# Kernel tuning notes

Measured on AMD Instinct MI355X. Metric: run time of the kernel, lower is better.

The kernel has to match this reference:

```python
import jax, jax.numpy as jnp
import numpy as np
from math import factorial

AGG_NORM = 10.0

def _cg(l1, m1, l2, m2, l3, m3):
    if m3 != m1 + m2:
        return 0.0
    f = factorial
    pre = ((2*l3+1) * f(l3+l1-l2) * f(l3-l1+l2) * f(l1+l2-l3) / f(l1+l2+l3+1)) ** 0.5
    pre *= (f(l3+m3)*f(l3-m3)*f(l1-m1)*f(l1+m1)*f(l2-m2)*f(l2+m2)) ** 0.5
    s = 0.0
    for k in range(0, l1+l2-l3+1):
        d = [k, l1+l2-l3-k, l1-m1-k, l2+m2-k, l3-l2+m1+k, l3-l1-m2+k]
        if min(d) < 0:
            continue
        s += (-1.0)**k / np.prod([float(f(x)) for x in d])
    return pre * s

def _U(l):
    U = np.zeros((2*l+1, 2*l+1), dtype=complex)
    U[l, l] = 1.0
    s2 = 2 ** -0.5
    for m in range(1, l+1):
        U[l+m, l+m] = (-1)**m * s2
        U[l+m, l-m] = s2
        U[l-m, l-m] = 1j * s2
        U[l-m, l+m] = -1j * (-1)**m * s2
    return U

def _real_w3j(l1, l2, l3):
    w = np.zeros((2*l1+1, 2*l2+1, 2*l3+1))
    for m1 in range(-l1, l1+1):
        for m2 in range(-l2, l2+1):
            m3 = -(m1+m2)
            if abs(m3) <= l3:
                w[m1+l1, m2+l2, m3+l3] = (-1.0)**(l1-l2-m3) * _cg(l1, m1, l2, m2, l3, -m3) / (2*l3+1) ** 0.5
    R = np.einsum('im,jn,ko,mno->ijk', _U(l1), _U(l2), _U(l3), w.astype(complex))
    R = R.real if np.abs(R.real).max() >= np.abs(R.imag).max() else R.imag
    return jnp.asarray((R / np.linalg.norm(R)).astype(np.float32))

_TRIPLES = [(0,0,0),(0,1,1),(0,2,2),(1,0,1),(1,1,0),(1,1,2),(1,2,1),(2,0,2),(2,1,1),(2,2,0),(2,2,2),(2,2,4)]
W3J = {t: _real_w3j(*t) for t in _TRIPLES}
PATHS1 = [(0,0,0),(0,1,1),(0,2,2)]
PATHS2 = [(0,0,0),(0,1,1),(0,2,2),(1,0,1),(1,1,0),(1,1,2),(1,2,1),(2,0,2),(2,1,1),(2,2,0),(2,2,2)]
PATHS_P = [(0,0,0),(0,2,2),(2,0,2),(2,2,0),(2,2,2)]
PATHS_4 = [(0,0,0),(2,2,0),(0,2,2),(2,0,2),(2,2,2),(2,2,4)]

def _cart_basis():
    # 21-dim orthonormal basis of rank-4 tensors with ijkl=ijlk=jikl=klij symmetry
    pairs = [(0,0),(1,1),(2,2),(1,2),(0,2),(0,1)]
    mats = []
    for i, j in pairs:
        A = np.zeros((3,3)); A[i,j] = 1.0; A[j,i] = 1.0
        mats.append(A / np.linalg.norm(A))
    B = []
    for a in range(6):
        for b in range(a, 6):
            T = 0.5*(np.einsum('ij,kl->ijkl', mats[a], mats[b]) + np.einsum('ij,kl->ijkl', mats[b], mats[a]))
            B.append(T / np.linalg.norm(T))
    return jnp.asarray(np.stack(B).astype(np.float32))
B21 = _cart_basis()
_MI = np.array([0,1,2,1,0,0]); _MJ = np.array([0,1,2,2,2,1])
_MF = jnp.asarray(np.array([1,1,1,2**0.5,2**0.5,2**0.5], dtype=np.float32))

def _sh(u):
    # component-normalized real spherical harmonics, l=0..2
    x, y, z = u[:,0], u[:,1], u[:,2]
    s0 = jnp.ones_like(x)[:, None]
    s1 = 3**0.5 * u
    s2 = jnp.stack([15**0.5*x*y, 15**0.5*y*z, 5**0.5/2*(3*z*z-1), 15**0.5*x*z, 15**0.5/2*(x*x-y*y)], axis=1)
    return [s0, s1, s2]

def _gauss(x, start, end, n):
    v = jnp.linspace(start, end, n)
    step = (end - start) / (n - 1)
    return jnp.exp(-(((x[:, None] - v) / step) ** 2)) / 1.12

def _lin(x, w):
    return jnp.einsum('nck,cd->ndk', x, w)

def _interaction(xs, sh, ef, senders, receivers, n_nodes, up_w, m1, m2, lin_w, lin_b, paths, norm):
    ups = [None if x is None else _lin(x, up_w[i]) for i, x in enumerate(xs)]
    E = ef.shape[0]
    w = (jax.nn.silu(ef @ m1) @ m2).reshape(E, len(paths), -1)
    gath = {l: ups[l][senders] for l in range(len(ups)) if ups[l] is not None}
    msgs = {}
    for p, (l1, l2, l3) in enumerate(paths):
        m = jnp.einsum('eci,ej,ijk,ec->eck', gath[l1], sh[l2], W3J[(l1, l2, l3)], w[:, p, :])
        msgs[l3] = msgs[l3] + m if l3 in msgs else m
    out = []
    for l in (0, 1, 2):
        agg = jax.ops.segment_sum(msgs[l], receivers, num_segments=n_nodes) / norm
        y = _lin(agg, lin_w[l])
        if l == 0:
            y = y + lin_b[None, :, None]
        out.append(y)
    return out

def _ctp(a, b, pw):
    out = {}
    for p, (l1, l2, l3) in enumerate(PATHS_P):
        m = jnp.einsum('gci,gcj,ijk,c->gck', a[l1], b[l2], W3J[(l1, l2, l3)], pw[p])
        out[l3] = out[l3] + m if l3 in out else m
    return out

def _forward(positions, node_attrs, edge_attr, shifts, W_embed, b_embed, up1_w, mlp1_w1, mlp1_w2, lin1_w, lin1_b, up2_w, mlp2_w1, mlp2_w2, lin2_w, lin2_b, ro_lin_w, ro_gate_w, ro_gate_b, ro_lin2_w, glin_w0, glin_b0, glin_w2, prod_pw2, prod_pw3, prod_lin, fo_w, edge_index, batch, num_graphs):
    N = positions.shape[0]
    senders, receivers = edge_index[0], edge_index[1]
    x0 = (node_attrs @ W_embed + b_embed)[:, :, None]            # [N,64,1]
    vec = positions[receivers] - positions[senders] + shifts
    length = jnp.linalg.norm(vec, axis=1, keepdims=True)
    sh = _sh(vec / (length + 1e-9))
    ef = jnp.concatenate([_gauss(length[:, 0], 0.0, 0.6, 6), _gauss(edge_attr[:, 0], 0.0, 0.03, 6)], axis=1)
    xs = _interaction([x0], sh, ef, senders, receivers, N, up1_w, mlp1_w1, mlp1_w2, lin1_w, lin1_b, PATHS1, AGG_NORM)
    xs = _interaction(xs, sh, ef, senders, receivers, N, up2_w, mlp2_w1, mlp2_w2, lin2_w, lin2_b, PATHS2, AGG_NORM)
    h = [_lin(xs[l], ro_lin_w[l]) for l in range(3)]
    gates = jax.nn.silu(xs[0][:, :, 0] @ ro_gate_w + ro_gate_b)  # [N,128]
    y0 = jax.nn.silu(h[0]); y1 = h[1] * gates[:, :64, None]; y2 = h[2] * gates[:, 64:, None]
    y = [_lin(a, ro_lin2_w[i]) for i, a in enumerate((y0, y1, y2))]
    cnt = jnp.clip(jax.ops.segment_sum(jnp.ones((N,), y[0].dtype), batch, num_segments=num_graphs), 1.0)
    g = [jax.ops.segment_sum(a, batch, num_segments=num_graphs) / cnt[:, None, None] for a in y]
    r = {0: _lin(g[0], glin_w0) + glin_b0[None, :, None], 2: _lin(g[2], glin_w2)}
    t2 = _ctp(r, r, prod_pw2)
    t3 = _ctp(t2, r, prod_pw3)
    r = {l: _lin(r[l], prod_lin[0, i]) + _lin(t2[l], prod_lin[1, i]) + _lin(t3[l], prod_lin[2, i]) for i, l in enumerate((0, 2))}
    outs = {}
    for p, (l1, l2, l3) in enumerate(PATHS_4):
        wp = fo_w[p][:, :, :1] if l3 == 4 else fo_w[p]
        m = jnp.einsum('gui,gvj,ijk,uvw->gwk', r[l1], r[l2], W3J[(l1, l2, l3)], wp)
        outs[l3] = outs[l3] + m if l3 in outs else m
    G = outs[0].shape[0]
    v = jnp.concatenate([outs[0].reshape(G, 2), outs[2].reshape(G, 10), outs[4].reshape(G, 9)], axis=1)
    stiff = jnp.einsum('ga,aijkl->gijkl', v, B21)
    C = stiff[:, _MI[:, None], _MJ[:, None], _MI[None, :], _MJ[None, :]] * (_MF[:, None] * _MF[None, :])
    return C @ C  # matrix_func = 'square'

def setup_inputs():
    k = jax.random.split(jax.random.key(0), 32)
    N, E, G, C = 20000, 200000, 128, 64
    s = lambda i, shape, sc=1.0: jax.random.normal(k[i], shape, dtype=jnp.float32) * sc
    return {
        'positions': jax.random.uniform(k[0], (N, 3), dtype=jnp.float32),
        'node_attrs': jax.random.uniform(k[1], (N, 1), dtype=jnp.float32),
        'edge_attr': jax.random.uniform(k[2], (E, 1), dtype=jnp.float32) * 0.03,
        'shifts': jnp.zeros((E, 3), jnp.float32),
        'W_embed': s(5, (1, C)),
        'b_embed': jnp.zeros((C,), jnp.float32),
        'up1_w': s(6, (1, C, C), C**-0.5),
        'mlp1_w1': s(7, (12, C), 12**-0.5),
        'mlp1_w2': s(8, (C, 3 * C), C**-0.5),
        'lin1_w': s(9, (3, C, C), C**-0.5),
        'lin1_b': jnp.zeros((C,), jnp.float32),
        'up2_w': s(10, (3, C, C), C**-0.5),
        'mlp2_w1': s(11, (12, C), 12**-0.5),
        'mlp2_w2': s(12, (C, 11 * C), C**-0.5),
        'lin2_w': s(13, (3, C, C), C**-0.5),
        'lin2_b': jnp.zeros((C,), jnp.float32),
        'ro_lin_w': s(14, (3, C, C), C**-0.5),
        'ro_gate_w': s(15, (C, 2 * C), C**-0.5),
        'ro_gate_b': jnp.zeros((2 * C,), jnp.float32),
        'ro_lin2_w': s(16, (3, C, C), C**-0.5),
        'glin_w0': s(17, (C, 16), C**-0.5),
        'glin_b0': jnp.zeros((16,), jnp.float32),
        'glin_w2': s(18, (C, 16), C**-0.5),
        'prod_pw2': s(19, (5, 16), 0.5),
        'prod_pw3': s(20, (5, 16), 0.5),
        'prod_lin': s(21, (3, 2, 16, 16), 0.25),
        'fo_w': s(22, (6, 16, 16, 2), 0.25),
        'edge_index': jax.random.randint(k[3], (2, E), 0, N),
        'batch': jnp.sort(jax.random.randint(k[4], (N,), 0, G)),
        'num_graphs': G,
    }

def reference(positions, node_attrs, edge_attr, shifts, W_embed, b_embed, up1_w, mlp1_w1, mlp1_w2, lin1_w, lin1_b, up2_w, mlp2_w1, mlp2_w2, lin2_w, lin2_b, ro_lin_w, ro_gate_w, ro_gate_b, ro_lin2_w, glin_w0, glin_b0, glin_w2, prod_pw2, prod_pw3, prod_lin, fo_w, edge_index, batch, num_graphs):
    return _forward(positions, node_attrs, edge_attr, shifts, W_embed, b_embed, up1_w, mlp1_w1, mlp1_w2, lin1_w, lin1_b, up2_w, mlp2_w1, mlp2_w2, lin2_w, lin2_b, ro_lin_w, ro_gate_w, ro_gate_b, ro_lin2_w, glin_w0, glin_b0, glin_w2, prod_pw2, prod_pw3, prod_lin, fo_w, edge_index, batch, num_graphs)
```

## Files before the change

kernel.cpp:

```cpp
#include <hip/hip_runtime.h>
#include <cmath>
#include <complex>
#include <vector>
#include <cstring>

static double hfact(int n){ double r=1; for(int i=2;i<=n;i++) r*=i; return r; }

static double hcg(int l1,int m1,int l2,int m2,int l3,int m3){
  if(m3!=m1+m2) return 0.0;
  double pre = std::sqrt((2*l3+1)*hfact(l3+l1-l2)*hfact(l3-l1+l2)*hfact(l1+l2-l3)/hfact(l1+l2+l3+1));
  pre *= std::sqrt(hfact(l3+m3)*hfact(l3-m3)*hfact(l1-m1)*hfact(l1+m1)*hfact(l2-m2)*hfact(l2+m2));
  double s=0;
  for(int k=0;k<=l1+l2-l3;k++){
    int d0=k,d1=l1+l2-l3-k,d2=l1-m1-k,d3=l2+m2-k,d4=l3-l2+m1+k,d5=l3-l1-m2+k;
    if(d0<0||d1<0||d2<0||d3<0||d4<0||d5<0) continue;
    double den=hfact(d0)*hfact(d1)*hfact(d2)*hfact(d3)*hfact(d4)*hfact(d5);
    s += ((k&1)?-1.0:1.0)/den;
  }
  return pre*s;
}

static void hU(int l, std::complex<double>* U){
  int n=2*l+1;
  for(int i=0;i<n*n;i++) U[i]=std::complex<double>(0.0,0.0);
  U[l*n+l]=1.0;
  double s2=std::sqrt(0.5);
  for(int m=1;m<=l;m++){
    double sgn=(m&1)?-1.0:1.0;
    U[(l+m)*n+(l+m)] = sgn*s2;
    U[(l+m)*n+(l-m)] = s2;
    U[(l-m)*n+(l-m)] = std::complex<double>(0.0, s2);
    U[(l-m)*n+(l+m)] = std::complex<double>(0.0, -sgn*s2);
  }
}

static void real_w3j(int l1,int l2,int l3, float* out){
  int n1=2*l1+1,n2=2*l2+1,n3=2*l3+1;
  std::vector<double> w((size_t)n1*n2*n3,0.0);
  for(int m1=-l1;m1<=l1;m1++)for(int m2=-l2;m2<=l2;m2++){
    int m3=-(m1+m2);
    if(m3<-l3||m3>l3) continue;
    int e=l1-l2-m3;
    double sgn = (((e%2)+2)%2)?-1.0:1.0;
    w[((size_t)(m1+l1)*n2+(m2+l2))*n3+(m3+l3)] = sgn*hcg(l1,m1,l2,m2,l3,-m3)/std::sqrt((double)(2*l3+1));
  }
  std::vector<std::complex<double>> U1((size_t)n1*n1),U2((size_t)n2*n2),U3((size_t)n3*n3),R((size_t)n1*n2*n3,std::complex<double>(0,0));
  hU(l1,U1.data()); hU(l2,U2.data()); hU(l3,U3.data());
  for(int i=0;i<n1;i++)for(int j=0;j<n2;j++)for(int k=0;k<n3;k++){
    std::complex<double> acc(0.0,0.0);
    for(int m=0;m<n1;m++){
      std::complex<double> u1=U1[i*n1+m]; if(u1.real()==0.0&&u1.imag()==0.0) continue;
      for(int nn=0;nn<n2;nn++){
        std::complex<double> u2=U2[j*n2+nn]; if(u2.real()==0.0&&u2.imag()==0.0) continue;
        std::complex<double> u12=u1*u2;
        for(int o=0;o<n3;o++){
          double wv=w[((size_t)m*n2+nn)*n3+o];
          if(wv!=0.0) acc += u12*U3[k*n3+o]*wv;
        }
      }
    }
    R[((size_t)i*n2+j)*n3+k]=acc;
  }
  double mre=0,mim=0;
  for(size_t t=0;t<R.size();t++){ mre=std::max(mre,std::fabs(R[t].real())); mim=std::max(mim,std::fabs(R[t].imag())); }
  bool useRe = (mre>=mim);
  double nrm=0;
  for(size_t t=0;t<R.size();t++){ double v=useRe?R[t].real():R[t].imag(); nrm+=v*v; }
  nrm=std::sqrt(nrm);
  for(size_t t=0;t<R.size();t++){ double v=useRe?R[t].real():R[t].imag(); out[t]=(float)(v/nrm); }
}

struct WAll {
  float w000;
  float w011[9];
  float w022[25];
  float w101[9];
  float w110[9];
  float w112[45];
  float w121[45];
  float w202[25];
  float w211[45];
  float w220[25];
  float w222[125];
};
struct Wg { float w000; float w022[25]; float w202[25]; float w220[25]; float w222[125]; float w224[225]; };

__device__ __forceinline__ float bcast(float v, int l){
  return __int_as_float(__builtin_amdgcn_readlane(__float_as_int(v), l));
}
__device__ __forceinline__ float silu(float x){ return x/(1.f+expf(-x)); }

__global__ __launch_bounds__(256) void k_prep(
  const float* __restrict__ We, const float* __restrict__ be, const float* __restrict__ up1,
  const float* __restrict__ lin1, const float* __restrict__ lin1b, const float* __restrict__ up2,
  float* __restrict__ M123, float* __restrict__ Svec, float* __restrict__ Tvec, float* __restrict__ bias2)
{
  int idx=blockIdx.x*256+threadIdx.x;
  if(idx<12288){
    int l=idx>>12, c=(idx>>6)&63, d=idx&63;
    float a=0;
    for(int k=0;k<64;k++) a+=lin1[l*4096+c*64+k]*up2[l*4096+k*64+d];
    M123[idx]=0.1f*a;
  } else if(idx<12352){
    int d=idx-12288; float a=0;
    for(int c=0;c<64;c++) a+=We[c]*up1[c*64+d];
    Svec[d]=a;
  } else if(idx<12416){
    int d=idx-12352; float a=0;
    for(int c=0;c<64;c++) a+=be[c]*up1[c*64+d];
    Tvec[d]=a;
  } else if(idx<12480){
    int d=idx-12416; float a=0;
    for(int c=0;c<64;c++) a+=lin1b[c]*up2[c*64+d];
    bias2[d]=a;
  }
}

__global__ __launch_bounds__(256) void k_shuf(
  const float* __restrict__ w2a, const float* __restrict__ w2b,
  float* __restrict__ T1, float* __restrict__ T2)
{
  int idx=blockIdx.x*256+threadIdx.x;
  if(idx<16384){
    int p=idx&3, c=(idx>>2)&63, h=idx>>8;
    T1[idx]=(p<3)? w2a[h*192+p*64+c] : 0.f;
  } else if(idx<16384+49152){
    int q2=idx-16384;
    int h=q2/768, rem=q2%768, qq=rem>>8, rem2=rem&255, c=rem2>>2, j=rem2&3;
    int p=qq*4+j;
    T2[q2]=(p<11)? w2b[h*704+p*64+c] : 0.f;
  }
}

__global__ __launch_bounds__(256) void k_hist(const int* __restrict__ eidx, int* __restrict__ hist, int E){
  int e=blockIdx.x*256+threadIdx.x;
  if(e<E) atomicAdd(&hist[eidx[E+e]], 1);
}

__global__ __launch_bounds__(256) void k_scan(int* __restrict__ ho, int N){
  __shared__ int tsum[256];
  int tid=threadIdx.x;
  int chunk=(N+255)/256;
  int lo=tid*chunk; if(lo>N) lo=N;
  int hi=lo+chunk; if(hi>N) hi=N;
  int s=0;
  for(int i=lo;i<hi;i++) s+=ho[i];
  tsum[tid]=s;
  __syncthreads();
  for(int off=1;off<256;off<<=1){
    int add=(tid>=off)? tsum[tid-off]:0;
    __syncthreads();
    tsum[tid]+=add;
    __syncthreads();
  }
  int base=(tid==0)?0:tsum[tid-1];
  for(int i=lo;i<hi;i++){
    int v=ho[i];
    ho[i]=base;
    base+=v;
  }
}

__global__ __launch_bounds__(256) void k_scatter(
  const int* __restrict__ eidx, int* __restrict__ offs,
  int* __restrict__ posOf, int* __restrict__ sndS, int* __restrict__ rcvS, int E)
{
  int e=blockIdx.x*256+threadIdx.x;
  if(e<E){
    int r=eidx[E+e];
    int pos=atomicAdd(&offs[r],1);
    posOf[e]=pos;
    sndS[pos]=eidx[e];
    rcvS[pos]=r;
  }
}

__global__ __launch_bounds__(256) void k_geom(
  const float* __restrict__ pos, const float* __restrict__ shifts,
  const float* __restrict__ eattr, const int* __restrict__ eidx,
  const int* __restrict__ posOf,
  float* __restrict__ shb, float* __restrict__ efb, float* __restrict__ Tbl,
  int E, WAll W)
{
  int e=blockIdx.x*256+threadIdx.x;
  if(e>=E) return;
  int s=eidx[e], r=eidx[E+e];
  int ps=posOf[e];
  float vx=pos[r*3+0]-pos[s*3+0]+shifts[e*3+0];
  float vy=pos[r*3+1]-pos[s*3+1]+shifts[e*3+1];
  float vz=pos[r*3+2]-pos[s*3+2]+shifts[e*3+2];
  float len=sqrtf(vx*vx+vy*vy+vz*vz);
  float inv=1.f/(len+1e-9f);
  float x=vx*inv,y=vy*inv,z=vz*inv;
  const float c3=1.7320508075688772f, c15=3.872983346207417f, c5h=1.118033988749895f, c15h=1.9364916731037085f;
  float s1[3]={c3*x, c3*y, c3*z};
  float s2[5]={c15*x*y, c15*y*z, c5h*(3.f*z*z-1.f), c15*x*z, c15h*(x*x-y*y)};
  float* sp=&shb[(size_t)ps*12];
  sp[0]=1.f; sp[1]=s1[0]; sp[2]=s1[1]; sp[3]=s1[2];
  sp[4]=s2[0]; sp[5]=s2[1]; sp[6]=s2[2]; sp[7]=s2[3]; sp[8]=s2[4];
  sp[9]=0.f; sp[10]=0.f; sp[11]=0.f;
  float ea=eattr[e];
  float* fp=&efb[(size_t)ps*12];
  #pragma unroll
  for(int i=0;i<6;i++){ float d=(len-0.12f*(float)i)/0.12f; fp[i]=expf(-d*d)/1.12f; }
  #pragma unroll
  for(int i=0;i<6;i++){ float d=(ea-0.006f*(float)i)/0.006f; fp[6+i]=expf(-d*d)/1.12f; }
  if(Tbl){
    float* tb=&Tbl[(size_t)ps*96];
    #pragma unroll
    for(int k=0;k<3;k++) tb[k]=s1[k]*W.w011[k*4];
    tb[3]=0.f;
    #pragma unroll
    for(int k=0;k<5;k++) tb[4+k]=s2[k]*W.w022[k*6];
    tb[9]=0.f; tb[10]=0.f; tb[11]=0.f;
    #pragma unroll
    for(int i=0;i<3;i++) tb[12+i]=s1[i]*W.w110[i*4];
    tb[15]=0.f;
    #pragma unroll
    for(int i=0;i<5;i++) tb[16+i]=s2[i]*W.w220[i*6];
    tb[21]=0.f; tb[22]=0.f; tb[23]=0.f;
    #pragma unroll
    for(int i=0;i<3;i++)
      #pragma unroll
      for(int k=0;k<3;k++){ float t=0;
        #pragma unroll
        for(int j=0;j<5;j++) t+=s2[j]*W.w121[(i*5+j)*3+k];
        tb[24+i*3+k]=t; }
    tb[33]=0.f; tb[34]=0.f; tb[35]=0.f;
    #pragma unroll
    for(int i=0;i<5;i++)
      #pragma unroll
      for(int k=0;k<3;k++){ float t=0;
        #pragma unroll
        for(int j=0;j<3;j++) t+=s1[j]*W.w211[(i*3+j)*3+k];
        tb[36+i*3+k]=t; }
    tb[51]=0.f;
    #pragma unroll
    for(int i=0;i<3;i++)
      #pragma unroll
      for(int k=0;k<5;k++){ float t=0;
        #pragma unroll
        for(int j=0;j<3;j++) t+=s1[j]*W.w112[(i*3+j)*5+k];
        tb[52+i*5+k]=t; }
    tb[67]=0.f;
    #pragma unroll
    for(int i=0;i<5;i++)
      #pragma unroll
      for(int k=0;k<5;k++){ float t=0;
        #pragma unroll
        for(int j=0;j<5;j++) t+=s2[j]*W.w222[(i*5+j)*5+k];
        tb[68+i*5+k]=t; }
    tb[93]=0.f; tb[94]=0.f; tb[95]=0.f;
  }
}

template<int TBL>
__global__ __launch_bounds__(256) void k_edge1(
  const float* __restrict__ na, const float* __restrict__ SV, const float* __restrict__ TV,
  const float* __restrict__ m1, const float* __restrict__ m2T,
  const float* __restrict__ sh, const float* __restrict__ Tbl, const float* __restrict__ ef,
  const int* __restrict__ sndS, const int* __restrict__ rcvS,
  float* __restrict__ agg, int E, WAll W)
{
  __shared__ __align__(16) float wl[8*256];
  __shared__ float m1s[768];
  int tid=threadIdx.x, lane=tid&63, wid=tid>>6;
  for(int i=tid;i<768;i+=256) m1s[i]=m1[i];
  float Sv=SV[lane], Tv=TV[lane];
  __syncthreads();
  int nb=(E+31)/32;
  for(int b=blockIdx.x;b<nb;b+=gridDim.x){
    int e0=b*32+wid*8;
    float hid[8]; float acc[8][3];
    #pragma unroll
    for(int e=0;e<8;e++){
      float h=0.f;
      if(e0+e<E){
        const float4* fp=(const float4*)(ef+(size_t)(e0+e)*12);
        float4 f0=fp[0], f1=fp[1], f2=fp[2];
        h = f0.x*m1s[0*64+lane]+f0.y*m1s[1*64+lane]+f0.z*m1s[2*64+lane]+f0.w*m1s[3*64+lane]
          + f1.x*m1s[4*64+lane]+f1.y*m1s[5*64+lane]+f1.z*m1s[6*64+lane]+f1.w*m1s[7*64+lane]
          + f2.x*m1s[8*64+lane]+f2.y*m1s[9*64+lane]+f2.z*m1s[10*64+lane]+f2.w*m1s[11*64+lane];
      }
      hid[e]=silu(h);
      acc[e][0]=0; acc[e][1]=0; acc[e][2]=0;
    }
    for(int ch=0;ch<8;ch++){
      __syncthreads();
      const float4* src=(const float4*)(m2T+(size_t)ch*2048);
      float4* dst4=(float4*)wl;
      dst4[tid]=src[tid];
      dst4[tid+256]=src[tid+256];
      __syncthreads();
      #pragma unroll
      for(int h8=0;h8<8;h8++){
        int h=ch*8+h8;
        float4 mv=*(const float4*)&wl[(h8*64+lane)*4];
        #pragma unroll
        for(int e=0;e<8;e++){
          float s=bcast(hid[e],h);
          acc[e][0]+=s*mv.x; acc[e][1]+=s*mv.y; acc[e][2]+=s*mv.z;
        }
      }
    }
    float carry[9];
    #pragma unroll
    for(int k=0;k<9;k++) carry[k]=0.f;
    int lastR=-1;
    #pragma unroll
    for(int e=0;e<8;e++){
      int ee=e0+e;
      if(ee>=E) break;
      int snd=sndS[ee], rcv=rcvS[ee];
      if(lastR>=0 && rcv!=lastR){
        float* dst=&agg[(size_t)lastR*576];
        atomicAdd(&dst[lane], carry[0]);
        #pragma unroll
        for(int k=0;k<3;k++) atomicAdd(&dst[(1+k)*64+lane], carry[1+k]);
        #pragma unroll
        for(int k=0;k<5;k++) atomicAdd(&dst[(4+k)*64+lane], carry[4+k]);
        #pragma unroll
        for(int k=0;k<9;k++) carry[k]=0.f;
      }
      float g0 = na[snd]*Sv + Tv;
      if constexpr(TBL){
        const float* tb=&Tbl[(size_t)ee*96];
        carry[0]+=g0*W.w000*acc[e][0];
        #pragma unroll
        for(int k=0;k<3;k++) carry[1+k]+=g0*acc[e][1]*tb[k];
        #pragma unroll
        for(int k=0;k<5;k++) carry[4+k]+=g0*acc[e][2]*tb[4+k];
      } else {
        const float4* shp=(const float4*)(sh+(size_t)ee*12);
        float4 h0=shp[0], h1=shp[1], h2=shp[2];
        float s1[3]={h0.y,h0.z,h0.w};
        float s2[5]={h1.x,h1.y,h1.z,h1.w,h2.x};
        carry[0]+=g0*W.w000*acc[e][0];
        #pragma unroll
        for(int k=0;k<3;k++) carry[1+k]+=g0*acc[e][1]*s1[k]*W.w011[k*4];
        #pragma unroll
        for(int k=0;k<5;k++) carry[4+k]+=g0*acc[e][2]*s2[k]*W.w022[k*6];
      }
      lastR=rcv;
    }
    if(lastR>=0){
      float* dst=&agg[(size_t)lastR*576];
      atomicAdd(&dst[lane], carry[0]);
      #pragma unroll
      for(int k=0;k<3;k++) atomicAdd(&dst[(1+k)*64+lane], carry[1+k]);
      #pragma unroll
      for(int k=0;k<5;k++) atomicAdd(&dst[(4+k)*64+lane], carry[4+k]);
    }
  }
}

template<int TBL>
__global__ __launch_bounds__(256) void k_edge2(
  const float* __restrict__ ups2, const float* __restrict__ m1, const float* __restrict__ m2T,
  const float* __restrict__ sh, const float* __restrict__ Tbl, const float* __restrict__ ef,
  const int* __restrict__ sndS, const int* __restrict__ rcvS,
  float* __restrict__ agg, int E, WAll W)
{
  __shared__ __align__(16) float wl[8*768];
  __shared__ float m1s[768];
  int tid=threadIdx.x, lane=tid&63, wid=tid>>6;
  for(int i=tid;i<768;i+=256) m1s[i]=m1[i];
  __syncthreads();
  int nb=(E+15)/16;
  for(int b=blockIdx.x;b<nb;b+=gridDim.x){
    int e0=b*16+wid*4;
    float hid[4]; float acc[4][11];
    #pragma unroll
    for(int e=0;e<4;e++){
      float h=0.f;
      if(e0+e<E){
        const float4* fp=(const float4*)(ef+(size_t)(e0+e)*12);
        float4 f0=fp[0], f1=fp[1], f2=fp[2];
        h = f0.x*m1s[0*64+lane]+f0.y*m1s[1*64+lane]+f0.z*m1s[2*64+lane]+f0.w*m1s[3*64+lane]
          + f1.x*m1s[4*64+lane]+f1.y*m1s[5*64+lane]+f1.z*m1s[6*64+lane]+f1.w*m1s[7*64+lane]
          + f2.x*m1s[8*64+lane]+f2.y*m1s[9*64+lane]+f2.z*m1s[10*64+lane]+f2.w*m1s[11*64+lane];
      }
      hid[e]=silu(h);
      #pragma unroll
      for(int p=0;p<11;p++) acc[e][p]=0.f;
    }
    for(int ch=0;ch<8;ch++){
      __syncthreads();
      const float4* src=(const float4*)(m2T+(size_t)ch*6144);
      float4* dst4=(float4*)wl;
      #pragma unroll
      for(int i=0;i<6;i++) dst4[tid+i*256]=src[tid+i*256];
      __syncthreads();
      #pragma unroll
      for(int h8=0;h8<8;h8++){
        int h=ch*8+h8;
        float4 q0=*(const float4*)&wl[((h8*3+0)*64+lane)*4];
        float4 q1=*(const float4*)&wl[((h8*3+1)*64+lane)*4];
        float4 q2=*(const float4*)&wl[((h8*3+2)*64+lane)*4];
        #pragma unroll
        for(int e=0;e<4;e++){
          float s=bcast(hid[e],h);
          acc[e][0]+=s*q0.x; acc[e][1]+=s*q0.y; acc[e][2]+=s*q0.z; acc[e][3]+=s*q0.w;
          acc[e][4]+=s*q1.x; acc[e][5]+=s*q1.y; acc[e][6]+=s*q1.z; acc[e][7]+=s*q1.w;
          acc[e][8]+=s*q2.x; acc[e][9]+=s*q2.y; acc[e][10]+=s*q2.z;
        }
      }
    }
    float carry[9];
    #pragma unroll
    for(int k=0;k<9;k++) carry[k]=0.f;
    int lastR=-1;
    #pragma unroll
    for(int e=0;e<4;e++){
      int ee=e0+e;
      if(ee>=E) break;
      int snd=sndS[ee], rcv=rcvS[ee];
      if(lastR>=0 && rcv!=lastR){
        float* dst=&agg[(size_t)lastR*576];
        atomicAdd(&dst[lane], carry[0]);
        #pragma unroll
        for(int k=0;k<3;k++) atomicAdd(&dst[(1+k)*64+lane], carry[1+k]);
        #pragma unroll
        for(int k=0;k<5;k++) atomicAdd(&dst[(4+k)*64+lane], carry[4+k]);
        #pragma unroll
        for(int k=0;k<9;k++) carry[k]=0.f;
      }
      const float* up=&ups2[(size_t)snd*576];
      float a0=acc[e][0],a1=acc[e][1],a2=acc[e][2],a3=acc[e][3];
      float a4=acc[e][4],a5=acc[e][5],a6=acc[e][6],a7=acc[e][7];
      float a8=acc[e][8],a9=acc[e][9],a10=acc[e][10];
      float g0=up[lane];
      float g1[3], g2[5];
      #pragma unroll
      for(int i=0;i<3;i++) g1[i]=up[(1+i)*64+lane];
      #pragma unroll
      for(int i=0;i<5;i++) g2[i]=up[(4+i)*64+lane];
      if constexpr(TBL){
        const float* tb=&Tbl[(size_t)ee*96];
        {
          float t110 = g1[0]*tb[12]+g1[1]*tb[13]+g1[2]*tb[14];
          float t220 = g2[0]*tb[16]+g2[1]*tb[17]+g2[2]*tb[18]+g2[3]*tb[19]+g2[4]*tb[20];
          carry[0] += W.w000*g0*a0 + a4*t110 + a9*t220;
        }
        #pragma unroll
        for(int k=0;k<3;k++){
          float t121 = g1[0]*tb[24+k]+g1[1]*tb[27+k]+g1[2]*tb[30+k];
          float t211 = g2[0]*tb[36+k]+g2[1]*tb[39+k]+g2[2]*tb[42+k]+g2[3]*tb[45+k]+g2[4]*tb[48+k];
          carry[1+k] += g0*a1*tb[k] + a3*g1[k]*W.w101[k*4] + a6*t121 + a8*t211;
        }
        #pragma unroll
        for(int k=0;k<5;k++){
          float t112 = g1[0]*tb[52+k]+g1[1]*tb[57+k]+g1[2]*tb[62+k];
          float t222 = g2[0]*tb[68+k]+g2[1]*tb[73+k]+g2[2]*tb[78+k]+g2[3]*tb[83+k]+g2[4]*tb[88+k];
          carry[4+k] += g0*a2*tb[4+k] + a7*g2[k]*W.w202[k*6] + a5*t112 + a10*t222;
        }
      } else {
        const float4* shp=(const float4*)(sh+(size_t)ee*12);
        float4 h0=shp[0], h1=shp[1], h2=shp[2];
        float s1[3]={h0.y,h0.z,h0.w};
        float s2[5]={h1.x,h1.y,h1.z,h1.w,h2.x};
        {
          float t110 = g1[0]*s1[0]*W.w110[0]+g1[1]*s1[1]*W.w110[4]+g1[2]*s1[2]*W.w110[8];
          float t220 = 0;
          #pragma unroll
          for(int i=0;i<5;i++) t220 += g2[i]*s2[i]*W.w220[i*6];
          carry[0] += W.w000*g0*a0 + a4*t110 + a9*t220;
        }
        #pragma unroll
        for(int k=0;k<3;k++){
          float mk = g0*a1*s1[k]*W.w011[k*4];
          mk += a3*g1[k]*W.w101[k*4];
          float t=0;
          #pragma unroll
          for(int i=0;i<3;i++){ float u=0;
            #pragma unroll
            for(int j=0;j<5;j++) u+=s2[j]*W.w121[(i*5+j)*3+k];
            t+=g1[i]*u; }
          mk += a6*t;
          t=0;
          #pragma unroll
          for(int i=0;i<5;i++){ float u=0;
            #pragma unroll
            for(int j=0;j<3;j++) u+=s1[j]*W.w211[(i*3+j)*3+k];
            t+=g2[i]*u; }
          mk += a8*t;
          carry[1+k]+=mk;
        }
        #pragma unroll
        for(int k=0;k<5;k++){
          float mk = g0*a2*s2[k]*W.w022[k*6];
          float t=0;
          #pragma unroll
          for(int i=0;i<3;i++){ float u=0;
            #pragma unroll
            for(int j=0;j<3;j++) u+=s1[j]*W.w112[(i*3+j)*5+k];
            t+=g1[i]*u; }
          mk += a5*t;
          mk += a7*g2[k]*W.w202[k*6];
          t=0;
          #pragma unroll
          for(int i=0;i<5;i++){ float u=0;
            #pragma unroll
            for(int j=0;j<5;j++) u+=s2[j]*W.w222[(i*5+j)*5+k];
            t+=g2[i]*u; }
          mk += a10*t;
          carry[4+k]+=mk;
        }
      }
      lastR=rcv;
    }
    if(lastR>=0){
      float* dst=&agg[(size_t)lastR*576];
      atomicAdd(&dst[lane], carry[0]);
      #pragma unroll
      for(int k=0;k<3;k++) atomicAdd(&dst[(1+k)*64+lane], carry[1+k]);
      #pragma unroll
      for(int k=0;k<5;k++) atomicAdd(&dst[(4+k)*64+lane], carry[4+k]);
    }
  }
}

template<int MODE>
__global__ __launch_bounds__(256) void k_node(
  const float* __restrict__ X, float* __restrict__ Y,
  const float* __restrict__ Ms, const float* __restrict__ bias,
  const float* __restrict__ gates, const int* __restrict__ batch,
  int N, float scale)
{
  int kk=blockIdx.y;
  int l=(kk==0)?0:(kk<4)?1:2;
  __shared__ float Mt[64][68];
  const float* M=Ms+l*4096;
  int tid=threadIdx.x;
  for(int idx=tid;idx<4096;idx+=256){ int c=idx>>6,d=idx&63; Mt[d][c]=M[idx]; }
  __syncthreads();
  int lane=tid&63, wid=tid>>6;
  int n0=(blockIdx.x*4+wid)*4;
  float xr[4];
  #pragma unroll
  for(int t=0;t<4;t++){ int n=n0+t; xr[t]=(n<N)?X[(size_t)n*576+kk*64+lane]:0.f; }
  float acc[4]={0,0,0,0};
  for(int cb=0;cb<64;cb+=4){
    float4 mv=*(const float4*)&Mt[lane][cb];
    #pragma unroll
    for(int t=0;t<4;t++){
      acc[t]+=bcast(xr[t],cb+0)*mv.x;
      acc[t]+=bcast(xr[t],cb+1)*mv.y;
      acc[t]+=bcast(xr[t],cb+2)*mv.z;
      acc[t]+=bcast(xr[t],cb+3)*mv.w;
    }
  }
  #pragma unroll
  for(int t=0;t<4;t++){
    int n=n0+t; if(n>=N) break;
    float v=acc[t]*scale;
    if constexpr(MODE==0||MODE==1){
      if(kk==0) v+=bias[lane];
      Y[(size_t)n*576+kk*64+lane]=v;
    } else if constexpr(MODE==2){
      if(kk==0) v=silu(v);
      else if(kk<4) v*=gates[(size_t)n*128+lane];
      else v*=gates[(size_t)n*128+64+lane];
      Y[(size_t)n*576+kk*64+lane]=v;
    } else {
      int bg=batch[n];
      atomicAdd(&Y[(size_t)bg*576+kk*64+lane], v);
    }
  }
}

__global__ __launch_bounds__(256) void k_gates(
  const float* __restrict__ xs, const float* __restrict__ gw, const float* __restrict__ gb,
  float* __restrict__ gates, int N)
{
  __shared__ float Gt[128][68];
  int tid=threadIdx.x;
  for(int idx=tid; idx<8192; idx+=256){ int c=idx>>7, t=idx&127; Gt[t][c]=gw[c*128+t]; }
  __syncthreads();
  int lane=tid&63, wid=tid>>6;
  int n0=(blockIdx.x*4+wid)*4;
  float xr[4];
  #pragma unroll
  for(int t=0;t<4;t++){ int n=n0+t; xr[t]=(n<N)?xs[(size_t)n*576+lane]:0.f; }
  float a0[4]={0,0,0,0}, a1[4]={0,0,0,0};
  for(int cb=0;cb<64;cb+=4){
    float4 m0=*(const float4*)&Gt[lane][cb];
    float4 m1=*(const float4*)&Gt[64+lane][cb];
    #pragma unroll
    for(int t=0;t<4;t++){
      float x0=bcast(xr[t],cb), x1=bcast(xr[t],cb+1), x2=bcast(xr[t],cb+2), x3=bcast(xr[t],cb+3);
      a0[t]+=x0*m0.x+x1*m0.y+x2*m0.z+x3*m0.w;
      a1[t]+=x0*m1.x+x1*m1.y+x2*m1.z+x3*m1.w;
    }
  }
  #pragma unroll
  for(int t=0;t<4;t++){
    int n=n0+t; if(n>=N) break;
    float g0=a0[t]+gb[lane], g1=a1[t]+gb[64+lane];
    gates[(size_t)n*128+lane]=silu(g0);
    gates[(size_t)n*128+64+lane]=silu(g1);
  }
}

__global__ __launch_bounds__(256) void k_cnt(const int* __restrict__ batch, float* __restrict__ cnt, int N){
  int n=blockIdx.x*256+threadIdx.x;
  if(n<N) atomicAdd(&cnt[batch[n]], 1.f);
}

__device__ void ctp_dev(const float* a0, const float* a2, const float* b0, const float* b2,
                        const float* pw, float* o0, float* o2, int c, const Wg& W)
{
  float A0=a0[c], B0=b0[c], A2[5], B2[5];
  #pragma unroll
  for(int i=0;i<5;i++){ A2[i]=a2[c*5+i]; B2[i]=b2[c*5+i]; }
  float o = pw[0*16+c]*A0*B0*W.w000;
  { float t=0;
    #pragma unroll
    for(int i=0;i<5;i++)
      #pragma unroll
      for(int j=0;j<5;j++) t+=A2[i]*B2[j]*W.w220[i*5+j];
    o += pw[3*16+c]*t; }
  o0[c]=o;
  #pragma unroll
  for(int k=0;k<5;k++){
    float t=0;
    { float s=0;
      #pragma unroll
      for(int j=0;j<5;j++) s+=B2[j]*W.w022[j*5+k];
      t+=pw[1*16+c]*A0*s; }
    { float s=0;
      #pragma unroll
      for(int i=0;i<5;i++) s+=A2[i]*W.w202[i*5+k];
      t+=pw[2*16+c]*s*B0; }
    { float s=0;
      #pragma unroll
      for(int i=0;i<5;i++)
        #pragma unroll
        for(int j=0;j<5;j++) s+=A2[i]*B2[j]*W.w222[(i*5+j)*5+k];
      t+=pw[4*16+c]*s; }
    o2[c*5+k]=t;
  }
}

__global__ __launch_bounds__(256) void k_graph(
  const float* __restrict__ gsum, const float* __restrict__ cnt,
  const float* __restrict__ glin_w0, const float* __restrict__ glin_b0, const float* __restrict__ glin_w2,
  const float* __restrict__ pw2, const float* __restrict__ pw3, const float* __restrict__ PL,
  const float* __restrict__ fo_w, float* __restrict__ out, Wg W)
{
  int g=blockIdx.x, tid=threadIdx.x;
  __shared__ float g0[64], g2[64*5];
  __shared__ float r0[16], r2[16*5];
  __shared__ float t20[16], t22[16*5];
  __shared__ float t30[16], t32[16*5];
  __shared__ float rp0[16], rp2[16*5];
  __shared__ float outs0[2], outs2[10], outs4[9];
  __shared__ float vv[21], stf[81], Cm[36];
  __shared__ float B21s[21*81];

  if(tid<21){
    const int pi[6]={0,1,2,1,0,0}, pj[6]={0,1,2,2,2,1};
    int a=0,b=0,idx=tid;
    for(a=0;a<6;a++){ int c6=6-a; if(idx<c6){ b=a+idx; break; } idx-=c6; }
    float ma[9]; float mb[9];
    for(int x=0;x<9;x++){ ma[x]=0; mb[x]=0; }
    { float v=(pi[a]==pj[a])?1.f:0.7071067811865476f; ma[pi[a]*3+pj[a]]=v; ma[pj[a]*3+pi[a]]=v; }
    { float v=(pi[b]==pj[b])?1.f:0.7071067811865476f; mb[pi[b]*3+pj[b]]=v; mb[pj[b]*3+pi[b]]=v; }
    float T[81]; float nrm=0;
    for(int x=0;x<81;x++){
      int ij=x/9, kl=x%9;
      float t=0.5f*(ma[ij]*mb[kl]+mb[ij]*ma[kl]);
      T[x]=t; nrm+=t*t;
    }
    nrm=sqrtf(nrm);
    for(int x=0;x<81;x++) B21s[tid*81+x]=T[x]/nrm;
  }

  float cinv=1.f/fmaxf(cnt[g],1.f);
  if(tid<64){
    g0[tid]=gsum[(size_t)g*576+tid]*cinv;
    for(int k=0;k<5;k++) g2[tid*5+k]=gsum[(size_t)g*576+(4+k)*64+tid]*cinv;
  }
  __syncthreads();

  if(tid<16){
    float a=0;
    for(int c=0;c<64;c++) a+=g0[c]*glin_w0[c*16+tid];
    r0[tid]=a+glin_b0[tid];
  } else if(tid<96){
    int u=(tid-16)/5, k=(tid-16)%5; float a=0;
    for(int c=0;c<64;c++) a+=g2[c*5+k]*glin_w2[c*16+u];
    r2[u*5+k]=a;
  }
  __syncthreads();

  if(tid<16) ctp_dev(r0,r2, r0,r2, pw2, t20,t22, tid, W);
  __syncthreads();
  if(tid<16) ctp_dev(t20,t22, r0,r2, pw3, t30,t32, tid, W);
  __syncthreads();

  if(tid<16){
    int d=tid; float a=0;
    for(int c=0;c<16;c++)
      a += r0[c]*PL[(0*2+0)*256+c*16+d] + t20[c]*PL[(1*2+0)*256+c*16+d] + t30[c]*PL[(2*2+0)*256+c*16+d];
    rp0[d]=a;
  } else if(tid<96){
    int q=tid-16, d=q/5, k=q%5; float a=0;
    for(int c=0;c<16;c++)
      a += r2[c*5+k]*PL[(0*2+1)*256+c*16+d] + t22[c*5+k]*PL[(1*2+1)*256+c*16+d] + t32[c*5+k]*PL[(2*2+1)*256+c*16+d];
    rp2[d*5+k]=a;
  }
  if(tid<2) outs0[tid]=0.f;
  else if(tid<12) outs2[tid-2]=0.f;
  else if(tid<21) outs4[tid-12]=0.f;
  __syncthreads();

  {
    int u=tid>>4, v=tid&15;
    float A0=rp0[u], B0=rp0[v], A2[5], B2[5];
    #pragma unroll
    for(int i=0;i<5;i++){ A2[i]=rp2[u*5+i]; B2[i]=rp2[v*5+i]; }
    float s00 = A0*B0*W.w000;
    float s220=0;
    #pragma unroll
    for(int i=0;i<5;i++)
      #pragma unroll
      for(int j=0;j<5;j++) s220+=A2[i]*B2[j]*W.w220[i*5+j];
    float s022[5], s202[5], s222[5], s224[9];
    #pragma unroll
    for(int k=0;k<5;k++){
      float s=0;
      #pragma unroll
      for(int j=0;j<5;j++) s+=B2[j]*W.w022[j*5+k];
      s022[k]=A0*s;
      float s2v=0;
      #pragma unroll
      for(int i=0;i<5;i++) s2v+=A2[i]*W.w202[i*5+k];
      s202[k]=s2v*B0;
      float s3v=0;
      #pragma unroll
      for(int i=0;i<5;i++)
        #pragma unroll
        for(int j=0;j<5;j++) s3v+=A2[i]*B2[j]*W.w222[(i*5+j)*5+k];
      s222[k]=s3v;
    }
    #pragma unroll
    for(int k=0;k<9;k++){
      float s=0;
      #pragma unroll
      for(int i=0;i<5;i++)
        #pragma unroll
        for(int j=0;j<5;j++) s+=A2[i]*B2[j]*W.w224[(i*5+j)*9+k];
      s224[k]=s;
    }
    #pragma unroll
    for(int w=0;w<2;w++){
      float f0=fo_w[((0*16+u)*16+v)*2+w], f1=fo_w[((1*16+u)*16+v)*2+w];
      float f2=fo_w[((2*16+u)*16+v)*2+w], f3=fo_w[((3*16+u)*16+v)*2+w];
      float f4=fo_w[((4*16+u)*16+v)*2+w];
      atomicAdd(&outs0[w], s00*f0 + s220*f1);
      #pragma unroll
      for(int k=0;k<5;k++)
        atomicAdd(&outs2[w*5+k], s022[k]*f2 + s202[k]*f3 + s222[k]*f4);
    }
    float f5=fo_w[((5*16+u)*16+v)*2+0];
    #pragma unroll
    for(int k=0;k<9;k++) atomicAdd(&outs4[k], s224[k]*f5);
  }
  __syncthreads();

  if(tid<2) vv[tid]=outs0[tid];
  else if(tid<12) vv[tid]=outs2[tid-2];
  else if(tid<21) vv[tid]=outs4[tid-12];
  __syncthreads();
  if(tid<81){
    float a=0;
    for(int q=0;q<21;q++) a+=vv[q]*B21s[q*81+tid];
    stf[tid]=a;
  }
  __syncthreads();
  {
    const int MI[6]={0,1,2,1,0,0}, MJ[6]={0,1,2,2,2,1};
    const float MF[6]={1.f,1.f,1.f,1.4142135623730951f,1.4142135623730951f,1.4142135623730951f};
    if(tid<36){
      int p=tid/6, q=tid%6;
      Cm[tid]=stf[MI[p]*27+MJ[p]*9+MI[q]*3+MJ[q]]*MF[p]*MF[q];
    }
  }
  __syncthreads();
  if(tid<36){
    int p=tid/6, q=tid%6; float a=0;
    for(int r=0;r<6;r++) a+=Cm[p*6+r]*Cm[r*6+q];
    out[(size_t)g*36+tid]=a;
  }
}

extern "C" void kernel_launch(void* const* d_in, const int* in_sizes, int n_in,
                              void* d_out, int out_size, void* d_ws, size_t ws_size,
                              hipStream_t stream)
{
  const float* positions=(const float*)d_in[0];
  const float* node_attrs=(const float*)d_in[1];
  const float* edge_attr=(const float*)d_in[2];
  const float* shifts=(const float*)d_in[3];
  const float* W_embed=(const float*)d_in[4];
  const float* b_embed=(const float*)d_in[5];
  const float* up1_w=(const float*)d_in[6];
  const float* mlp1_w1=(const float*)d_in[7];
  const float* mlp1_w2=(const float*)d_in[8];
  const float* lin1_w=(const float*)d_in[9];
  const float* lin1_b=(const float*)d_in[10];
  const float* up2_w=(const float*)d_in[11];
  const float* mlp2_w1=(const float*)d_in[12];
  const float* mlp2_w2=(const float*)d_in[13];
  const float* lin2_w=(const float*)d_in[14];
  const float* lin2_b=(const float*)d_in[15];
  const float* ro_lin_w=(const float*)d_in[16];
  const float* ro_gate_w=(const float*)d_in[17];
  const float* ro_gate_b=(const float*)d_in[18];
  const float* ro_lin2_w=(const float*)d_in[19];
  const float* glin_w0=(const float*)d_in[20];
  const float* glin_b0=(const float*)d_in[21];
  const float* glin_w2=(const float*)d_in[22];
  const float* prod_pw2=(const float*)d_in[23];
  const float* prod_pw3=(const float*)d_in[24];
  const float* prod_lin=(const float*)d_in[25];
  const float* fo_w=(const float*)d_in[26];
  const int* edge_index=(const int*)d_in[27];
  const int* batch=(const int*)d_in[28];
  const int N=in_sizes[1];
  const int E=in_sizes[2];
  const int G=128;
  float* out=(float*)d_out;

  float* p=(float*)d_ws;
  float* shb=p;    p+=(size_t)12*E;
  float* efb=p;    p+=(size_t)12*E;
  float* bufA=p;   p+=(size_t)N*576;
  float* bufB=p;   p+=(size_t)N*576;
  float* gatesb=p; p+=(size_t)N*128;
  float* M123=p;   p+=3*4096;
  float* Svec=p;   p+=64;
  float* Tvec=p;   p+=64;
  float* bias2=p;  p+=64;
  float* m2T1=p;   p+=16384;
  float* m2T2=p;   p+=49152;
  float* gsum=p;   p+=(size_t)G*576;
  float* cntb=p;   p+=G;
  int* offs=(int*)p;   p+=N;
  int* posOf=(int*)p;  p+=E;
  int* sndS=(int*)p;   p+=E;
  int* rcvS=(int*)p;   p+=E;
  size_t baseNeed=(size_t)(p-(float*)d_ws)*sizeof(float);
  if(baseNeed>ws_size) return;
  float* Tbl=p;
  bool useTbl = (baseNeed + (size_t)96*E*sizeof(float)) <= ws_size;
  if(!useTbl) Tbl=nullptr;

  WAll wa; Wg wg;
  {
    float t000[1],t011[9],t022[25],t101[9],t110[9],t112[45],t121[45],t202[25],t211[45],t220[25],t222[125],t224[225];
    real_w3j(0,0,0,t000); real_w3j(0,1,1,t011); real_w3j(0,2,2,t022);
    real_w3j(1,0,1,t101); real_w3j(1,1,0,t110); real_w3j(1,1,2,t112); real_w3j(1,2,1,t121);
    real_w3j(2,0,2,t202); real_w3j(2,1,1,t211); real_w3j(2,2,0,t220); real_w3j(2,2,2,t222); real_w3j(2,2,4,t224);
    wa.w000=t000[0];
    std::memcpy(wa.w011,t011,sizeof t011); std::memcpy(wa.w022,t022,sizeof t022);
    std::memcpy(wa.w101,t101,sizeof t101); std::memcpy(wa.w110,t110,sizeof t110);
    std::memcpy(wa.w112,t112,sizeof t112); std::memcpy(wa.w121,t121,sizeof t121);
    std::memcpy(wa.w202,t202,sizeof t202); std::memcpy(wa.w211,t211,sizeof t211);
    std::memcpy(wa.w220,t220,sizeof t220); std::memcpy(wa.w222,t222,sizeof t222);
    wg.w000=t000[0];
    std::memcpy(wg.w022,t022,sizeof t022); std::memcpy(wg.w202,t202,sizeof t202);
    std::memcpy(wg.w220,t220,sizeof t220); std::memcpy(wg.w222,t222,sizeof t222);
    std::memcpy(wg.w224,t224,sizeof t224);
  }

  k_prep<<<49,256,0,stream>>>(W_embed,b_embed,up1_w,lin1_w,lin1_b,up2_w,M123,Svec,Tvec,bias2);
  k_shuf<<<256,256,0,stream>>>(mlp1_w2,mlp2_w2,m2T1,m2T2);

  hipMemsetAsync(offs,0,(size_t)N*sizeof(int),stream);
  k_hist<<<(E+255)/256,256,0,stream>>>(edge_index,offs,E);
  k_scan<<<1,256,0,stream>>>(offs,N);
  k_scatter<<<(E+255)/256,256,0,stream>>>(edge_index,offs,posOf,sndS,rcvS,E);

  k_geom<<<(E+255)/256,256,0,stream>>>(positions,shifts,edge_attr,edge_index,posOf,shb,efb,Tbl,E,wa);

  hipMemsetAsync(bufA,0,(size_t)N*576*sizeof(float),stream);
  const int eblocks=1280;
  if(useTbl)
    k_edge1<1><<<eblocks,256,0,stream>>>(node_attrs,Svec,Tvec,mlp1_w1,m2T1,shb,Tbl,efb,sndS,rcvS,bufA,E,wa);
  else
    k_edge1<0><<<eblocks,256,0,stream>>>(node_attrs,Svec,Tvec,mlp1_w1,m2T1,shb,Tbl,efb,sndS,rcvS,bufA,E,wa);

  dim3 ngrid((N+15)/16,9);
  k_node<0><<<ngrid,256,0,stream>>>(bufA,bufB,M123,bias2,nullptr,nullptr,N,1.0f);

  hipMemsetAsync(bufA,0,(size_t)N*576*sizeof(float),stream);
  if(useTbl)
    k_edge2<1><<<eblocks,256,0,stream>>>(bufB,mlp2_w1,m2T2,shb,Tbl,efb,sndS,rcvS,bufA,E,wa);
  else
    k_edge2<0><<<eblocks,256,0,stream>>>(bufB,mlp2_w1,m2T2,shb,Tbl,efb,sndS,rcvS,bufA,E,wa);

  k_node<1><<<ngrid,256,0,stream>>>(bufA,bufB,lin2_w,lin2_b,nullptr,nullptr,N,0.1f);
  k_gates<<<(N+15)/16,256,0,stream>>>(bufB,ro_gate_w,ro_gate_b,gatesb,N);
  k_node<2><<<ngrid,256,0,stream>>>(bufB,bufA,ro_lin_w,nullptr,gatesb,nullptr,N,1.0f);

  hipMemsetAsync(gsum,0,((size_t)G*576+G)*sizeof(float),stream);
  k_cnt<<<(N+255)/256,256,0,stream>>>(batch,cntb,N);
  k_node<3><<<ngrid,256,0,stream>>>(bufA,gsum,ro_lin2_w,nullptr,nullptr,batch,N,1.0f);

  k_graph<<<G,256,0,stream>>>(gsum,cntb,glin_w0,glin_b0,glin_w2,prod_pw2,prod_pw3,prod_lin,fo_w,out,wg);
}
```

Baseline: 1.290 ms.

## Fuse lin2, gate computation and readout linear into one node kernel

```diff
diff --git a/kernel.cpp b/kernel.cpp
--- a/kernel.cpp
+++ b/kernel.cpp
@@ -569,36 +569,104 @@
   }
 }
 
-__global__ __launch_bounds__(256) void k_gates(
-  const float* __restrict__ xs, const float* __restrict__ gw, const float* __restrict__ gb,
-  float* __restrict__ gates, int N)
-{
-  __shared__ float Gt[128][68];
-  int tid=threadIdx.x;
-  for(int idx=tid; idx<8192; idx+=256){ int c=idx>>7, t=idx&127; Gt[t][c]=gw[c*128+t]; }
-  __syncthreads();
-  int lane=tid&63, wid=tid>>6;
+__global__ __launch_bounds__(256) void k_node_fused(
+  const float* __restrict__ X, float* __restrict__ Y,
+  const float* __restrict__ lin2, const float* __restrict__ lin2b,
+  const float* __restrict__ gw, const float* __restrict__ gb,
+  const float* __restrict__ rolin, int N)
+{
+  __shared__ float Wt[128][68];
+  int tid=threadIdx.x, lane=tid&63, wid=tid>>6;
   int n0=(blockIdx.x*4+wid)*4;
-  float xr[4];
+  float xs[4][9];
+  float b0=lin2b[lane];
   #pragma unroll
-  for(int t=0;t<4;t++){ int n=n0+t; xr[t]=(n<N)?xs[(size_t)n*576+lane]:0.f; }
-  float a0[4]={0,0,0,0}, a1[4]={0,0,0,0};
-  for(int cb=0;cb<64;cb+=4){
-    float4 m0=*(const float4*)&Gt[lane][cb];
-    float4 m1=*(const float4*)&Gt[64+lane][cb];
-    #pragma unroll
-    for(int t=0;t<4;t++){
-      float x0=bcast(xr[t],cb), x1=bcast(xr[t],cb+1), x2=bcast(xr[t],cb+2), x3=bcast(xr[t],cb+3);
-      a0[t]+=x0*m0.x+x1*m0.y+x2*m0.z+x3*m0.w;
-      a1[t]+=x0*m1.x+x1*m1.y+x2*m1.z+x3*m1.w;
-    }
+  for(int l=0;l<3;l++){
+    __syncthreads();
+    {
+      const float* M=lin2+l*4096;
+      for(int idx=tid;idx<4096;idx+=256){ int c=idx>>6,d=idx&63; Wt[d][c]=M[idx]; }
+    }
+    __syncthreads();
+    const int kk0 = (l==0)?0:(l==1)?1:4;
+    const int kk1 = (l==0)?1:(l==1)?4:9;
+    #pragma unroll
+    for(int kk=kk0;kk<kk1;kk++){
+      float xr[4];
+      #pragma unroll
+      for(int t=0;t<4;t++){ int n=n0+t; xr[t]=(n<N)?X[(size_t)n*576+kk*64+lane]:0.f; }
+      float acc[4]={0,0,0,0};
+      for(int cb=0;cb<64;cb+=4){
+        float4 mv=*(const float4*)&Wt[lane][cb];
+        #pragma unroll
+        for(int t=0;t<4;t++){
+          acc[t]+=bcast(xr[t],cb+0)*mv.x;
+          acc[t]+=bcast(xr[t],cb+1)*mv.y;
+          acc[t]+=bcast(xr[t],cb+2)*mv.z;
+          acc[t]+=bcast(xr[t],cb+3)*mv.w;
+        }
+      }
+      #pragma unroll
+      for(int t=0;t<4;t++){
+        float v=acc[t]*0.1f;
+        if(kk==0) v+=b0;
+        xs[t][kk]=v;
+      }
+    }
+  }
+  __syncthreads();
+  for(int idx=tid; idx<8192; idx+=256){ int c=idx>>7, t=idx&127; Wt[t][c]=gw[c*128+t]; }
+  __syncthreads();
+  float gA[4], gB[4];
+  {
+    float a0[4]={0,0,0,0}, a1[4]={0,0,0,0};
+    for(int cb=0;cb<64;cb+=4){
+      float4 m0=*(const float4*)&Wt[lane][cb];
+      float4 m1=*(const float4*)&Wt[64+lane][cb];
+      #pragma unroll
+      for(int t=0;t<4;t++){
+        float x0=bcast(xs[t][0],cb), x1=bcast(xs[t][0],cb+1), x2=bcast(xs[t][0],cb+2), x3=bcast(xs[t][0],cb+3);
+        a0[t]+=x0*m0.x+x1*m0.y+x2*m0.z+x3*m0.w;
+        a1[t]+=x0*m1.x+x1*m1.y+x2*m1.z+x3*m1.w;
+      }
+    }
+    float gb0=gb[lane], gb1=gb[64+lane];
+    #pragma unroll
+    for(int t=0;t<4;t++){ gA[t]=silu(a0[t]+gb0); gB[t]=silu(a1[t]+gb1); }
   }
   #pragma unroll
-  for(int t=0;t<4;t++){
-    int n=n0+t; if(n>=N) break;
-    float g0=a0[t]+gb[lane], g1=a1[t]+gb[64+lane];
-    gates[(size_t)n*128+lane]=silu(g0);
-    gates[(size_t)n*128+64+lane]=silu(g1);
+  for(int l=0;l<3;l++){
+    __syncthreads();
+    {
+      const float* M=rolin+l*4096;
+      for(int idx=tid;idx<4096;idx+=256){ int c=idx>>6,d=idx&63; Wt[d][c]=M[idx]; }
+    }
+    __syncthreads();
+    const int kk0 = (l==0)?0:(l==1)?1:4;
+    const int kk1 = (l==0)?1:(l==1)?4:9;
+    #pragma unroll
+    for(int kk=kk0;kk<kk1;kk++){
+      float acc[4]={0,0,0,0};
+      for(int cb=0;cb<64;cb+=4){
+        float4 mv=*(const float4*)&Wt[lane][cb];
+        #pragma unroll
+        for(int t=0;t<4;t++){
+          acc[t]+=bcast(xs[t][kk],cb+0)*mv.x;
+          acc[t]+=bcast(xs[t][kk],cb+1)*mv.y;
+          acc[t]+=bcast(xs[t][kk],cb+2)*mv.z;
+          acc[t]+=bcast(xs[t][kk],cb+3)*mv.w;
+        }
+      }
+      #pragma unroll
+      for(int t=0;t<4;t++){
+        int n=n0+t; if(n>=N) continue;
+        float v=acc[t];
+        if(kk==0) v=silu(v);
+        else if(kk<4) v*=gA[t];
+        else v*=gB[t];
+        Y[(size_t)n*576+kk*64+lane]=v;
+      }
+    }
   }
 }
 
@@ -901,9 +969,7 @@
   else
     k_edge2<0><<<eblocks,256,0,stream>>>(bufB,mlp2_w1,m2T2,shb,Tbl,efb,sndS,rcvS,bufA,E,wa);
 
-  k_node<1><<<ngrid,256,0,stream>>>(bufA,bufB,lin2_w,lin2_b,nullptr,nullptr,N,0.1f);
-  k_gates<<<(N+15)/16,256,0,stream>>>(bufB,ro_gate_w,ro_gate_b,gatesb,N);
-  k_node<2><<<ngrid,256,0,stream>>>(bufB,bufA,ro_lin_w,nullptr,gatesb,nullptr,N,1.0f);
+  k_node_fused<<<(N+15)/16,256,0,stream>>>(bufA,bufA,lin2_w,lin2_b,ro_gate_w,ro_gate_b,ro_lin_w,N);
 
   hipMemsetAsync(gsum,0,((size_t)G*576+G)*sizeof(float),stream);
   k_cnt<<<(N+255)/256,256,0,stream>>>(batch,cntb,N);
```

Result: slower. 1.604 ms (+24.4%).
